# Kernel optimization log

Measured on AMD Instinct MI355X. Metric: run time of the kernel, lower is better.

Reference implementation:

```python
import jax, jax.numpy as jnp
import numpy as np
from jax import lax

B, DIM, H, W = 8, 192, 128, 128
K = 7            # kernel_size
STRIDE = 1
PAD = 3          # kernel_size // 2
RED = 4          # reduction
HID = DIM // RED # 48
EPS = 1e-5       # BatchNorm eps


def setup_inputs() -> dict:
    key = jax.random.key(0)
    ks = jax.random.split(key, 4)
    return {
        "x": jax.random.normal(ks[0], (B, DIM, H, W), dtype=jnp.float32),
        # conv1: 1x1, no bias -> [out=HID, in=DIM]
        "w1": jax.random.normal(ks[1], (HID, DIM), dtype=jnp.float32) * 0.05,
        # BatchNorm2d(HID) eval-mode params / running stats
        "bn_gamma": jnp.ones((HID,), jnp.float32),
        "bn_beta": jnp.zeros((HID,), jnp.float32),
        "bn_mean": jnp.zeros((HID,), jnp.float32),
        "bn_var": jnp.ones((HID,), jnp.float32),
        # conv2: 1x1 -> [out=DIM*K*K, in=HID], with bias
        "w2": jax.random.normal(ks[2], (DIM * K * K, HID), dtype=jnp.float32) * 0.05,
        "b2": jnp.zeros((DIM * K * K,), jnp.float32),
        # depthwise output bias (self.bias)
        "bias": jax.random.normal(ks[3], (DIM,), dtype=jnp.float32) * 0.05,
    }


def reference(x, w1, bn_gamma, bn_beta, bn_mean, bn_var, w2, b2, bias):
    b, c, h, w = x.shape
    # SE-style weight generation: pool -> 1x1 conv -> BN -> ReLU -> 1x1 conv
    pooled = x.mean(axis=(2, 3))                          # [b, c]
    y = jnp.einsum('bc,oc->bo', pooled, w1)               # [b, HID]
    y = (y - bn_mean) * lax.rsqrt(bn_var + EPS) * bn_gamma + bn_beta
    y = jax.nn.relu(y)
    wdyn = jnp.einsum('bh,oh->bo', y, w2) + b2            # [b, c*K*K]
    wdyn = wdyn.reshape(b, c, K, K)                       # per-sample depthwise kernels

    # per-sample depthwise conv (equiv. to groups=b*dim batch-folded trick)
    def dw(xi, wi):  # xi: [c,h,w], wi: [c,K,K]
        return lax.conv_general_dilated(
            xi[None], wi[:, None],              # [1,c,h,w], [c,1,K,K] (OIHW)
            window_strides=(STRIDE, STRIDE),
            padding=[(PAD, PAD), (PAD, PAD)],
            feature_group_count=c)[0]

    out = jax.vmap(dw)(x, wdyn) + bias[None, :, None, None]
    return out
```

## Files before the change

### kernel.cpp

```cpp
#include <hip/hip_runtime.h>

#define BATCH 8
#define DIM 192
#define HH 128
#define WW 128
#define KS 7
#define PAD 3
#define HID 48
#define KK 49
#define BN_EPS 1e-5f

#define TILE_H 64
#define SROWS (TILE_H + KS - 1)
#define SW 136

__global__ __launch_bounds__(256) void pool_kernel(const float* __restrict__ x,
                                                   float* __restrict__ pooled) {
    const int bc = blockIdx.x;
    const float4* p = (const float4*)(x + (size_t)bc * HH * WW);
    const int t = threadIdx.x;
    float s = 0.f;
#pragma unroll
    for (int i = 0; i < 16; ++i) {
        float4 v = p[t + i * 256];
        s += (v.x + v.y) + (v.z + v.w);
    }
#pragma unroll
    for (int off = 32; off > 0; off >>= 1) s += __shfl_down(s, off, 64);
    __shared__ float wsum[4];
    const int wave = t >> 6, lane = t & 63;
    if (lane == 0) wsum[wave] = s;
    __syncthreads();
    if (t == 0) {
        float tot = (wsum[0] + wsum[1]) + (wsum[2] + wsum[3]);
        pooled[bc] = tot * (1.0f / (HH * WW));
    }
}

__global__ __launch_bounds__(256) void wgen_kernel(const float* __restrict__ pooled,
                                                   const float* __restrict__ w1,
                                                   const float* __restrict__ gamma,
                                                   const float* __restrict__ beta,
                                                   const float* __restrict__ mean,
                                                   const float* __restrict__ var,
                                                   const float* __restrict__ w2,
                                                   const float* __restrict__ b2,
                                                   float* __restrict__ wdyn) {
    __shared__ float pool_s[BATCH * DIM];
    __shared__ float y_s[BATCH * HID];
    const int t = threadIdx.x;
    for (int i = t; i < BATCH * DIM; i += 256) pool_s[i] = pooled[i];
    __syncthreads();
    for (int i = t; i < BATCH * HID; i += 256) {
        const int b = i / HID, h = i - b * HID;
        const float4* pr = (const float4*)(pool_s + b * DIM);
        const float4* wr = (const float4*)(w1 + (size_t)h * DIM);
        float acc = 0.f;
#pragma unroll
        for (int j = 0; j < DIM / 4; ++j) {
            float4 pv = pr[j], wv = wr[j];
            acc += pv.x * wv.x + pv.y * wv.y + pv.z * wv.z + pv.w * wv.w;
        }
        float yv = (acc - mean[h]) * rsqrtf(var[h] + BN_EPS) * gamma[h] + beta[h];
        y_s[i] = yv > 0.f ? yv : 0.f;
    }
    __syncthreads();
    const int o = blockIdx.x * 256 + t;
    const int b = o / (DIM * KK);
    const int ol = o - b * (DIM * KK);
    const float4* w2r = (const float4*)(w2 + (size_t)ol * HID);
    const float* yb = y_s + b * HID;
    float acc = b2[ol];
#pragma unroll
    for (int j = 0; j < HID / 4; ++j) {
        float4 wv = w2r[j];
        acc += yb[4 * j] * wv.x + yb[4 * j + 1] * wv.y +
               yb[4 * j + 2] * wv.z + yb[4 * j + 3] * wv.w;
    }
    wdyn[o] = acc;
}

__global__ __launch_bounds__(256) void dwconv_kernel(const float* __restrict__ x,
                                                     const float* __restrict__ wdyn,
                                                     const float* __restrict__ bias,
                                                     float* __restrict__ out) {
    __shared__ float smem[SROWS][SW];
    __shared__ float wk_s[KK];
    const int tile = blockIdx.x / (BATCH * DIM);
    const int bc = blockIdx.x - tile * (BATCH * DIM);
    const int c = bc % DIM;
    const int t = threadIdx.x;
    const int r0 = tile * TILE_H;

    if (t < KK) wk_s[t] = wdyn[(size_t)bc * KK + t];

    const float* xp = x + (size_t)bc * HH * WW;
    for (int idx = t; idx < SROWS * 32; idx += 256) {
        const int r = idx >> 5;
        const int c4 = idx & 31;
        const int gr = r0 - PAD + r;
        float4 v = make_float4(0.f, 0.f, 0.f, 0.f);
        if (gr >= 0 && gr < HH) v = ((const float4*)(xp + (size_t)gr * WW))[c4];
        *((float4*)&smem[r][4 + c4 * 4]) = v;
    }
    if (t < SROWS * 2) {
        const int r = t >> 1;
        float4* p = (float4*)&smem[r][(t & 1) ? 132 : 0];
        *p = make_float4(0.f, 0.f, 0.f, 0.f);
    }
    __syncthreads();

    float wreg[KK];
#pragma unroll
    for (int i = 0; i < KK; ++i) wreg[i] = wk_s[i];
    const float bv = bias[c];

    const int c4 = t & 31;
    const int strip = t >> 5;
    const int sbase = strip * 8;
    float* outp = out + (size_t)bc * HH * WW + (size_t)(r0 + sbase) * WW + c4 * 4;

    float acc[7][4];
#pragma unroll
    for (int i = 0; i < 7; ++i)
        acc[i][0] = acc[i][1] = acc[i][2] = acc[i][3] = 0.f;

#pragma unroll
    for (int ir = 0; ir < TILE_H / 8 + KS - 1; ++ir) {
        const float* srow = &smem[sbase + ir][0];
        const float4 f0 = ((const float4*)srow)[c4];
        const float4 f1 = ((const float4*)srow)[c4 + 1];
        const float4 f2 = ((const float4*)srow)[c4 + 2];
        const float v[12] = {f0.x, f0.y, f0.z, f0.w,
                             f1.x, f1.y, f1.z, f1.w,
                             f2.x, f2.y, f2.z, f2.w};
#pragma unroll
        for (int ky = 0; ky < KS; ++ky) {
            const int o = ir - ky;
            if (o >= 0 && o < 8) {
                float* a = acc[o % 7];
#pragma unroll
                for (int kx = 0; kx < KS; ++kx) {
                    const float wv = wreg[ky * KS + kx];
                    a[0] += wv * v[1 + kx];
                    a[1] += wv * v[2 + kx];
                    a[2] += wv * v[3 + kx];
                    a[3] += wv * v[4 + kx];
                }
            }
        }
        if (ir >= 6) {
            float* a = acc[(ir - 6) % 7];
            float4 o4 = make_float4(a[0] + bv, a[1] + bv, a[2] + bv, a[3] + bv);
            *((float4*)(outp + (size_t)(ir - 6) * WW)) = o4;
            a[0] = a[1] = a[2] = a[3] = 0.f;
        }
    }
}

extern "C" void kernel_launch(void* const* d_in, const int* in_sizes, int n_in,
                              void* d_out, int out_size, void* d_ws, size_t ws_size,
                              hipStream_t stream) {
    const float* x     = (const float*)d_in[0];
    const float* w1    = (const float*)d_in[1];
    const float* gamma = (const float*)d_in[2];
    const float* beta  = (const float*)d_in[3];
    const float* mean  = (const float*)d_in[4];
    const float* var   = (const float*)d_in[5];
    const float* w2    = (const float*)d_in[6];
    const float* b2    = (const float*)d_in[7];
    const float* bias  = (const float*)d_in[8];
    float* out = (float*)d_out;

    float* pooled = (float*)d_ws;
    float* wdyn   = pooled + BATCH * DIM;

    pool_kernel<<<BATCH * DIM, 256, 0, stream>>>(x, pooled);
    wgen_kernel<<<(BATCH * DIM * KK) / 256, 256, 0, stream>>>(
        pooled, w1, gamma, beta, mean, var, w2, b2, wdyn);
    dwconv_kernel<<<BATCH * DIM * 2, 256, 0, stream>>>(x, wdyn, bias, out);
}
```

Before: 244.7 us.

## Load depthwise conv tile directly into LDS via global_load_lds

The halo tile load now uses the AMD global-to-LDS direct load builtin instead of going through registers. The shared layout drops its padding columns, so horizontal boundaries are handled by predicated neighbor reads. Out-of-range rows are clamped on load and then zeroed after a barrier. Block indexing is also changed so the two row tiles of one channel are adjacent, which should help L2 reuse. The aim is less register traffic and fewer instructions in the load phase, at the cost of an extra barrier and branches in the compute loop.

```diff
diff --git a/kernel.cpp b/kernel.cpp
--- a/kernel.cpp
+++ b/kernel.cpp
@@ -12,7 +12,7 @@
 
 #define TILE_H 64
 #define SROWS (TILE_H + KS - 1)
-#define SW 136
+#define NSLOT (SROWS * (WW / 4))
 
 __global__ __launch_bounds__(256) void pool_kernel(const float* __restrict__ x,
                                                    float* __restrict__ pooled) {
@@ -84,29 +84,37 @@
                                                      const float* __restrict__ wdyn,
                                                      const float* __restrict__ bias,
                                                      float* __restrict__ out) {
-    __shared__ float smem[SROWS][SW];
+    __shared__ float smem[SROWS][WW];
     __shared__ float wk_s[KK];
-    const int tile = blockIdx.x / (BATCH * DIM);
-    const int bc = blockIdx.x - tile * (BATCH * DIM);
+    const int tile = blockIdx.x & 1;
+    const int bc = blockIdx.x >> 1;
     const int c = bc % DIM;
     const int t = threadIdx.x;
     const int r0 = tile * TILE_H;
 
     if (t < KK) wk_s[t] = wdyn[(size_t)bc * KK + t];
 
-    const float* xp = x + (size_t)bc * HH * WW;
-    for (int idx = t; idx < SROWS * 32; idx += 256) {
-        const int r = idx >> 5;
-        const int c4 = idx & 31;
-        const int gr = r0 - PAD + r;
-        float4 v = make_float4(0.f, 0.f, 0.f, 0.f);
-        if (gr >= 0 && gr < HH) v = ((const float4*)(xp + (size_t)gr * WW))[c4];
-        *((float4*)&smem[r][4 + c4 * 4]) = v;
+    const int slo = tile ? 0 : PAD * (WW / 4);
+    const int shi = tile ? (SROWS - PAD) * (WW / 4) : NSLOT;
+    const float* xbase = x + (size_t)bc * HH * WW + (ptrdiff_t)(r0 - PAD) * WW;
+
+#pragma unroll
+    for (int i = 0; i < (NSLOT + 255) / 256; ++i) {
+        const int s = t + i * 256;
+        if (s < NSLOT) {
+            int sc = s;
+            if (sc < slo) sc = slo;
+            if (sc >= shi) sc = shi - 4;
+            __builtin_amdgcn_global_load_lds(
+                (const __attribute__((address_space(1))) void*)(xbase + (size_t)sc * 4),
+                (__attribute__((address_space(3))) void*)((float*)smem + (size_t)s * 4),
+                16, 0, 0);
+        }
     }
-    if (t < SROWS * 2) {
-        const int r = t >> 1;
-        float4* p = (float4*)&smem[r][(t & 1) ? 132 : 0];
-        *p = make_float4(0.f, 0.f, 0.f, 0.f);
+    __syncthreads();
+    if (t < PAD * (WW / 4)) {
+        const int zslot = (tile ? (SROWS - PAD) * (WW / 4) : 0) + t;
+        ((float4*)smem)[zslot] = make_float4(0.f, 0.f, 0.f, 0.f);
     }
     __syncthreads();
 
@@ -127,10 +135,12 @@
 
 #pragma unroll
     for (int ir = 0; ir < TILE_H / 8 + KS - 1; ++ir) {
-        const float* srow = &smem[sbase + ir][0];
-        const float4 f0 = ((const float4*)srow)[c4];
-        const float4 f1 = ((const float4*)srow)[c4 + 1];
-        const float4 f2 = ((const float4*)srow)[c4 + 2];
+        const float4* row4 = (const float4*)&smem[sbase + ir][0];
+        const float4 f1 = row4[c4];
+        float4 f0 = make_float4(0.f, 0.f, 0.f, 0.f);
+        float4 f2 = make_float4(0.f, 0.f, 0.f, 0.f);
+        if (c4 > 0)  f0 = row4[c4 - 1];
+        if (c4 < 31) f2 = row4[c4 + 1];
         const float v[12] = {f0.x, f0.y, f0.z, f0.w,
                              f1.x, f1.y, f1.z, f1.w,
                              f2.x, f2.y, f2.z, f2.w};
```

Measured after the change: 239.0 us. -2.3%, faster.
